# Performance work log

Hardware: AMD Instinct MI355X
Metric: run time of the kernel (lower is better)

## Reference

```python
import jax, jax.numpy as jnp
import numpy as np

HEAD_DIM = 64
N_HEADS = 25
N_KV_HEADS = 5
WINDOW = 1024
N_META = 128
EPS = 1e-6
ROPE_BASE = 10000.0


def _rmsnorm(x, w):
    # per-head RMSNorm over last dim, computed in fp32 (matches HymbaRMSNorm)
    xf = x.astype(jnp.float32)
    var = jnp.mean(xf * xf, axis=-1, keepdims=True)
    return w * (xf * jax.lax.rsqrt(var + EPS)).astype(x.dtype)


def _rotate_half(x):
    x1, x2 = jnp.split(x, 2, axis=-1)
    return jnp.concatenate((-x2, x1), axis=-1)


def _rope_cos_sin(position_ids):
    # equivalent to indexing the cached cos/sin tables with position_ids
    inv_freq = 1.0 / (ROPE_BASE ** (jnp.arange(0, HEAD_DIM, 2, dtype=jnp.float32) / HEAD_DIM))
    freqs = position_ids.astype(jnp.float32)[..., None] * inv_freq  # [B,T,hd/2]
    emb = jnp.concatenate((freqs, freqs), axis=-1)                   # [B,T,hd]
    return jnp.cos(emb)[:, None], jnp.sin(emb)[:, None]              # [B,1,T,hd]


def setup_inputs() -> dict:
    key = jax.random.key(0)
    k1, k2, k3, k4, k5 = jax.random.split(key, 5)
    B, T = 2, 2048
    return {
        "query_states": jax.random.normal(k1, (B, T, N_HEADS * HEAD_DIM), dtype=jnp.float32),
        "key_states": jax.random.normal(k2, (B, T, N_KV_HEADS * HEAD_DIM), dtype=jnp.float32),
        "value_states": jax.random.normal(k3, (B, T, N_KV_HEADS * HEAD_DIM), dtype=jnp.float32),
        "q_norm_w": jax.random.uniform(k4, (HEAD_DIM,), dtype=jnp.float32, minval=0.5, maxval=1.5),
        "k_norm_w": jax.random.uniform(k5, (HEAD_DIM,), dtype=jnp.float32, minval=0.5, maxval=1.5),
        "position_ids": jnp.broadcast_to(jnp.arange(T, dtype=jnp.int32), (B, T)),
    }


def reference(query_states, key_states, value_states, q_norm_w, k_norm_w, position_ids):
    B, T, _ = query_states.shape
    # [B, H, T, hd]
    q = query_states.reshape(B, T, N_HEADS, HEAD_DIM).transpose(0, 2, 1, 3)
    k = key_states.reshape(B, T, N_KV_HEADS, HEAD_DIM).transpose(0, 2, 1, 3)
    v = value_states.reshape(B, T, N_KV_HEADS, HEAD_DIM).transpose(0, 2, 1, 3)

    # per-head QK RMSNorm
    q = _rmsnorm(q, q_norm_w)
    k = _rmsnorm(k, k_norm_w)

    # RoPE
    cos, sin = _rope_cos_sin(position_ids)
    q = q * cos + _rotate_half(q) * sin
    k = k * cos + _rotate_half(k) * sin

    # GQA: repeat each kv head num_heads // num_kv_heads times (consecutively)
    n_rep = N_HEADS // N_KV_HEADS
    k_e = jnp.repeat(k, n_rep, axis=1)
    v_e = jnp.repeat(v, n_rep, axis=1)

    scale = 1.0 / np.sqrt(HEAD_DIM)
    scores = jnp.einsum("bhqd,bhkd->bhqk", q, k_e) * scale

    # SWA mask: causal AND (in sliding window OR meta/memory token)
    q_idx = jnp.arange(T)[:, None]
    k_idx = jnp.arange(T)[None, :]
    attend = (k_idx <= q_idx) & ((k_idx >= q_idx - WINDOW + 1) | (k_idx < N_META))
    scores = jnp.where(attend, scores, -jnp.inf)

    attn_weights = jax.nn.softmax(scores, axis=-1)
    out = jnp.einsum("bhqk,bhkd->bhqd", attn_weights, v_e)
    return out.transpose(0, 2, 1, 3).reshape(B, T, N_HEADS * HEAD_DIM)
```

## Files before the change

### kernel.cpp

```cpp
#include <hip/hip_runtime.h>
#include <cmath>

typedef float  f32x4  __attribute__((ext_vector_type(4)));
typedef __bf16 bf16x8 __attribute__((ext_vector_type(8)));
typedef unsigned int u32x4 __attribute__((ext_vector_type(4)));
typedef unsigned int u32x2 __attribute__((ext_vector_type(2)));
typedef unsigned int   u32;
typedef unsigned short u16;

#define HEAD_DIM 64
#define N_HEADS  25
#define N_KV     5
#define WINDOW   1024
#define N_META   128
#define B_       2
#define T_       2048
#define QB       64
#define NTILES   (T_ / 64)
#define TILE_U32 2048
#define SM_BIAS  (-20.0f)

static __device__ __forceinline__ u16 bf16_bits(float f) {
  __bf16 h = (__bf16)f;
  return __builtin_bit_cast(u16, h);
}
static __device__ __forceinline__ u32 pack2(float lo, float hi) {
  return ((u32)bf16_bits(hi) << 16) | bf16_bits(lo);
}
static __device__ __forceinline__ float fexp2(float x) {
  return __builtin_amdgcn_exp2f(x);
}
static __device__ __forceinline__ void gload16(const u32* g, u32* l) {
  __builtin_amdgcn_global_load_lds((const __attribute__((address_space(1))) u32*)g,
                                   (__attribute__((address_space(3))) u32*)l, 16, 0, 0);
}

__global__ __launch_bounds__(256) void prep_k_kernel(
    const float* __restrict__ k_in, const float* __restrict__ k_w,
    const int* __restrict__ pos_ids, u32* __restrict__ k_ws)
{
  int gw   = (blockIdx.x * blockDim.x + threadIdx.x) >> 6;
  int lane = threadIdx.x & 63;
  if (gw >= B_ * T_ * N_KV) return;
  int kvh = gw % N_KV;
  int bt  = gw / N_KV;

  float x = k_in[(size_t)bt * (N_KV * HEAD_DIM) + kvh * HEAD_DIM + lane];
  float ss = x * x;
  #pragma unroll
  for (int off = 32; off; off >>= 1) ss += __shfl_xor(ss, off);
  float y = k_w[lane] * x * rsqrtf(ss * (1.f / 64.f) + 1e-6f);

  int   pos = pos_ids[bt];
  float ang = (float)pos * powf(10000.f, -(float)(lane & 31) * (1.f / 32.f));
  float c, s;
  sincosf(ang, &s, &c);
  float part = __shfl_xor(y, 32);
  float r = (lane < 32) ? (y * c - part * s) : (y * c + part * s);

  u16 mybits = bf16_bits(r);
  u32 pb = (u32)(u16)__shfl_xor((int)mybits, 1);
  u32 w  = (pb << 16) | mybits;
  int b = bt / T_, t = bt % T_;
  if (!(lane & 1)) {
    int c32 = lane >> 1;
    int kl = t & 63, tile = t >> 6;
    int sp = (c32 >> 2) ^ (kl & 7);
    k_ws[(((size_t)(b * N_KV + kvh) * NTILES + tile)) * TILE_U32 + kl * 32 + sp * 4 + (c32 & 3)] = w;
  }
}

__global__ __launch_bounds__(256) void prep_v_kernel(
    const float* __restrict__ v_in, u32* __restrict__ v_ws)
{
  int blk  = blockIdx.x;
  int tile = blk & (NTILES - 1);
  int bk   = blk >> 5;
  int kvh  = bk % N_KV, b = bk / N_KV;
  int t0   = tile * 64;
  int tid  = threadIdx.x;

  __shared__ u16 Tl[64][72];

  #pragma unroll
  for (int it = 0; it < 4; ++it) {
    int idx = it * 256 + tid;
    int kl = idx >> 4, dq = idx & 15;
    const float4 f = *(const float4*)&v_in[((size_t)(b * T_ + t0 + kl)) * (N_KV * HEAD_DIM) + kvh * HEAD_DIM + dq * 4];
    Tl[dq * 4 + 0][kl] = bf16_bits(f.x);
    Tl[dq * 4 + 1][kl] = bf16_bits(f.y);
    Tl[dq * 4 + 2][kl] = bf16_bits(f.z);
    Tl[dq * 4 + 3][kl] = bf16_bits(f.w);
  }
  __syncthreads();

  u32* outb = v_ws + (size_t)blk * TILE_U32;
  #pragma unroll
  for (int it = 0; it < 8; ++it) {
    int o = it * 256 + tid;
    int d = o >> 5, c = o & 31;
    u32 w = ((u32)Tl[d][2 * c + 1] << 16) | Tl[d][2 * c];
    int a = c >> 4, bs = (c >> 3) & 1, gp = (c >> 1) & 3, e = c & 1;
    int sp = (4 * a + gp) ^ (d & 7);
    outb[d * 32 + sp * 4 + 2 * bs + e] = w;
  }
}

__global__ __launch_bounds__(256, 4) void attn_kernel(
    const float* __restrict__ q_in, const float* __restrict__ q_w,
    const int* __restrict__ pos_ids,
    const u32* __restrict__ kws, const u32* __restrict__ vws,
    float* __restrict__ out)
{
  const int i  = blockIdx.x;
  const int x  = i & 7, k = i >> 3;
  const int gA = (5 * x) >> 2;
  const int a0 = 200 * x - 160 * gA;
  const int nB = 40 + a0;
  int grp, j_;
  if (k < nB) { grp = gA + 1; j_ = k; }
  else        { grp = gA;     j_ = a0 + (k - nB); }
  const int qt  = 31 - j_ / 5;
  const int hh  = j_ % 5;
  const int b   = grp / 5;
  const int kvh = grp % 5;
  const int h   = kvh * 5 + hh;
  const int qb  = qt * QB;
  const int tid = threadIdx.x, wid = tid >> 6, lane = tid & 63;
  const int l15 = lane & 15, g = lane >> 4;
  const int qrow0 = wid * 16;

  __shared__ u32 Ks[2 * TILE_U32];
  __shared__ u32 Vt[2 * TILE_U32];

  const int nt    = (qt <= 18) ? (qt + 1) : 19;
  const int shift = qt - 18;

  const size_t kvbase = ((size_t)(b * N_KV + kvh)) * NTILES * TILE_U32;
  const u32* kb = kws + kvbase;
  const u32* vb = vws + kvbase;

  #pragma unroll
  for (int j = 0; j < 4; ++j) {
    int ci = (wid << 2) | j;
    if (ci < 8) gload16(kb + ci * 256 + lane * 4, &Ks[ci * 256]);
    else        gload16(vb + (ci - 8) * 256 + lane * 4, &Vt[(ci - 8) * 256]);
  }

  {
    const int   jbase = (4 * l15) & 31;
    const float r32   = 0.74989420933f;
    float fr[4];
    fr[0] = powf(10000.f, -(float)jbase * (1.f / 32.f));
    fr[1] = fr[0] * r32; fr[2] = fr[1] * r32; fr[3] = fr[2] * r32;

    const int t0g = b * T_ + qb + qrow0;
    int pos_prev = pos_ids[t0g + g];
    float cc[4], sn[4], c4[4], s4[4];
    #pragma unroll
    for (int e = 0; e < 4; ++e) {
      sincosf((float)pos_prev * fr[e], &sn[e], &cc[e]);
      sincosf(4.f * fr[e], &s4[e], &c4[e]);
    }
    const float4 wv = *(const float4*)&q_w[4 * l15];
    #pragma unroll
    for (int it = 0; it < 4; ++it) {
      const int row = 4 * it + g;
      if (it) {
        int pos = pos_ids[t0g + row];
        if (__all(pos == pos_prev + 4)) {
          #pragma unroll
          for (int e = 0; e < 4; ++e) {
            float c2 = cc[e] * c4[e] - sn[e] * s4[e];
            sn[e] = sn[e] * c4[e] + cc[e] * s4[e];
            cc[e] = c2;
          }
        } else {
          #pragma unroll
          for (int e = 0; e < 4; ++e) sincosf((float)pos * fr[e], &sn[e], &cc[e]);
        }
        pos_prev = pos;
      }
      const float4 xv = *(const float4*)&q_in[((size_t)(t0g + row)) * (N_HEADS * HEAD_DIM) + h * HEAD_DIM + 4 * l15];
      float ss = xv.x * xv.x + xv.y * xv.y + xv.z * xv.z + xv.w * xv.w;
      ss += __shfl_xor(ss, 1); ss += __shfl_xor(ss, 2);
      ss += __shfl_xor(ss, 4); ss += __shfl_xor(ss, 8);
      const float rn = rsqrtf(ss * (1.f / 64.f) + 1e-6f);
      float y[4] = {wv.x * xv.x * rn, wv.y * xv.y * rn, wv.z * xv.z * rn, wv.w * xv.w * rn};
      float rv[4];
      #pragma unroll
      for (int e = 0; e < 4; ++e) {
        float part = __shfl_xor(y[e], 8);
        rv[e] = ((l15 < 8) ? (y[e] * cc[e] - part * sn[e])
                           : (y[e] * cc[e] + part * sn[e])) * 0.18033688f;
      }
      u32x2 w2;
      w2.x = pack2(rv[0], rv[1]);
      w2.y = pack2(rv[2], rv[3]);
      *(u32x2*)&Ks[TILE_U32 + (qrow0 + row) * 32 + 2 * l15] = w2;
    }
  }
  __syncthreads();

  bf16x8 qf[2];
  #pragma unroll
  for (int ks = 0; ks < 2; ++ks)
    qf[ks] = *(const bf16x8*)&Ks[TILE_U32 + (qrow0 + l15) * 32 + 16 * ks + 4 * g];
  __syncthreads();

  float l_part = 0.f;
  f32x4 acc_o[4];
  #pragma unroll
  for (int mt = 0; mt < 4; ++mt) acc_o[mt] = (f32x4)(0.f);

  const int q_abs = qb + qrow0 + l15;

  int buf = 0;
  for (int i2 = 0; i2 < nt; ++i2) {
    if (i2 + 1 < nt) {
      int tn = (qt <= 18 || i2 + 1 < 2) ? (i2 + 1) : (i2 + 1 + shift);
      const u32* kt = kb + (size_t)tn * TILE_U32;
      const u32* vt = vb + (size_t)tn * TILE_U32;
      u32* kd = &Ks[(buf ^ 1) * TILE_U32];
      u32* vd = &Vt[(buf ^ 1) * TILE_U32];
      #pragma unroll
      for (int j = 0; j < 4; ++j) {
        int ci = (wid << 2) | j;
        if (ci < 8) gload16(kt + ci * 256 + lane * 4, kd + ci * 256);
        else        gload16(vt + (ci - 8) * 256 + lane * 4, vd + (ci - 8) * 256);
      }
    }
    const int k0 = ((qt <= 18 || i2 < 2) ? i2 : i2 + shift) << 6;

    f32x4 accs[4];
    #pragma unroll
    for (int mt = 0; mt < 4; ++mt) accs[mt] = (f32x4)(SM_BIAS);
    #pragma unroll
    for (int ks = 0; ks < 2; ++ks) {
      #pragma unroll
      for (int mt = 0; mt < 4; ++mt) {
        bf16x8 kf = *(const bf16x8*)&Ks[buf * TILE_U32 + (16 * mt + l15) * 32 + (((4 * ks + g) ^ (l15 & 7)) << 2)];
        accs[mt] = __builtin_amdgcn_mfma_f32_16x16x32_bf16(kf, qf[ks], accs[mt], 0, 0, 0);
      }
    }

    const bool do_mask = (i2 == nt - 1) || (qt >= 18 && i2 == 2);
    if (do_mask) {
      #pragma unroll
      for (int mt = 0; mt < 4; ++mt)
        #pragma unroll
        for (int rg = 0; rg < 4; ++rg) {
          int key = k0 + 16 * mt + 4 * g + rg;
          bool ok = (key <= q_abs) && ((key >= q_abs - (WINDOW - 1)) || (key < N_META));
          accs[mt][rg] = ok ? accs[mt][rg] : -INFINITY;
        }
    }
    float rsum = 0.f;
    #pragma unroll
    for (int mt = 0; mt < 4; ++mt)
      #pragma unroll
      for (int rg = 0; rg < 4; ++rg) {
        float pi = fexp2(accs[mt][rg]);
        accs[mt][rg] = pi;
        rsum += pi;
      }
    l_part += rsum;

    #pragma unroll
    for (int ks2 = 0; ks2 < 2; ++ks2) {
      const int m0 = 2 * ks2, m1 = 2 * ks2 + 1;
      u32x4 aw;
      aw.x = pack2(accs[m0][0], accs[m0][1]);
      aw.y = pack2(accs[m0][2], accs[m0][3]);
      aw.z = pack2(accs[m1][0], accs[m1][1]);
      aw.w = pack2(accs[m1][2], accs[m1][3]);
      bf16x8 af = __builtin_bit_cast(bf16x8, aw);
      #pragma unroll
      for (int mt2 = 0; mt2 < 4; ++mt2) {
        bf16x8 vf = *(const bf16x8*)&Vt[buf * TILE_U32 + (16 * mt2 + l15) * 32 + (((4 * ks2 + g) ^ (l15 & 7)) << 2)];
        acc_o[mt2] = __builtin_amdgcn_mfma_f32_16x16x32_bf16(af, vf, acc_o[mt2], 0, 0, 0);
      }
    }

    __syncthreads();
    buf ^= 1;
  }

  float lsum = l_part;
  lsum += __shfl_xor(lsum, 16);
  lsum += __shfl_xor(lsum, 32);
  float l4[4];
  #pragma unroll
  for (int rg = 0; rg < 4; ++rg) l4[rg] = __shfl(lsum, 4 * g + rg);
  #pragma unroll
  for (int mt2 = 0; mt2 < 4; ++mt2)
    #pragma unroll
    for (int rg = 0; rg < 4; ++rg) {
      int t = qb + qrow0 + 4 * g + rg;
      out[((size_t)(b * T_ + t)) * (N_HEADS * HEAD_DIM) + h * HEAD_DIM + 16 * mt2 + l15] =
          acc_o[mt2][rg] / l4[rg];
    }
}

extern "C" void kernel_launch(void* const* d_in, const int* in_sizes, int n_in,
                              void* d_out, int out_size, void* d_ws, size_t ws_size,
                              hipStream_t stream) {
  const float* q   = (const float*)d_in[0];
  const float* k   = (const float*)d_in[1];
  const float* v   = (const float*)d_in[2];
  const float* qw  = (const float*)d_in[3];
  const float* kw  = (const float*)d_in[4];
  const int*   pos = (const int*)d_in[5];

  u32* kp = (u32*)d_ws;
  u32* vp = kp + (size_t)B_ * N_KV * NTILES * TILE_U32;
  float* outp = (float*)d_out;

  prep_k_kernel<<<5120, 256, 0, stream>>>(k, kw, pos, kp);
  prep_v_kernel<<<B_ * N_KV * NTILES, 256, 0, stream>>>(v, vp);
  attn_kernel<<<1600, 256, 0, stream>>>(q, qw, pos, kp, vp, outp);
}
```

Measured before the change: 60.85 us.

## Split attention tile 2x2 across waves over query and key halves

Each of the four waves now handles 32 query rows against one 32-key half of each tile, instead of 16 query rows against all 64 keys. Each K fragment read from LDS is reused for two query fragments, cutting LDS reads per MFMA for the score product. The price is an end-of-kernel reduction: waves owning the second key half write partial outputs and row sums to shared memory, the other waves add them and store the result. This also raises accumulator register use.

```diff
diff --git a/kernel.cpp b/kernel.cpp
--- a/kernel.cpp
+++ b/kernel.cpp
@@ -128,7 +128,7 @@
   const int qb  = qt * QB;
   const int tid = threadIdx.x, wid = tid >> 6, lane = tid & 63;
   const int l15 = lane & 15, g = lane >> 4;
-  const int qrow0 = wid * 16;
+  const int qw  = wid >> 1, kw = wid & 1;
 
   __shared__ u32 Ks[2 * TILE_U32];
   __shared__ u32 Vt[2 * TILE_U32];
@@ -154,7 +154,7 @@
     fr[0] = powf(10000.f, -(float)jbase * (1.f / 32.f));
     fr[1] = fr[0] * r32; fr[2] = fr[1] * r32; fr[3] = fr[2] * r32;
 
-    const int t0g = b * T_ + qb + qrow0;
+    const int t0g = b * T_ + qb + wid * 16;
     int pos_prev = pos_ids[t0g + g];
     float cc[4], sn[4], c4[4], s4[4];
     #pragma unroll
@@ -197,23 +197,27 @@
       u32x2 w2;
       w2.x = pack2(rv[0], rv[1]);
       w2.y = pack2(rv[2], rv[3]);
-      *(u32x2*)&Ks[TILE_U32 + (qrow0 + row) * 32 + 2 * l15] = w2;
+      *(u32x2*)&Ks[TILE_U32 + (wid * 16 + row) * 32 + 2 * l15] = w2;
     }
   }
   __syncthreads();
 
-  bf16x8 qf[2];
-  #pragma unroll
-  for (int ks = 0; ks < 2; ++ks)
-    qf[ks] = *(const bf16x8*)&Ks[TILE_U32 + (qrow0 + l15) * 32 + 16 * ks + 4 * g];
+  bf16x8 qf[2][2];
+  #pragma unroll
+  for (int qn = 0; qn < 2; ++qn)
+    #pragma unroll
+    for (int ks = 0; ks < 2; ++ks)
+      qf[qn][ks] = *(const bf16x8*)&Ks[TILE_U32 + (32 * qw + 16 * qn + l15) * 32 + 16 * ks + 4 * g];
   __syncthreads();
 
-  float l_part = 0.f;
-  f32x4 acc_o[4];
-  #pragma unroll
-  for (int mt = 0; mt < 4; ++mt) acc_o[mt] = (f32x4)(0.f);
-
-  const int q_abs = qb + qrow0 + l15;
+  float l_part[2] = {0.f, 0.f};
+  f32x4 acc_o[2][4];
+  #pragma unroll
+  for (int qn = 0; qn < 2; ++qn)
+    #pragma unroll
+    for (int mt = 0; mt < 4; ++mt) acc_o[qn][mt] = (f32x4)(0.f);
+
+  const int q_abs0 = qb + 32 * qw + l15;
 
   int buf = 0;
   for (int i2 = 0; i2 < nt; ++i2) {
@@ -232,53 +236,61 @@
     }
     const int k0 = ((qt <= 18 || i2 < 2) ? i2 : i2 + shift) << 6;
 
-    f32x4 accs[4];
-    #pragma unroll
-    for (int mt = 0; mt < 4; ++mt) accs[mt] = (f32x4)(SM_BIAS);
+    f32x4 accs[2][2];
+    #pragma unroll
+    for (int qn = 0; qn < 2; ++qn)
+      #pragma unroll
+      for (int mt = 0; mt < 2; ++mt) accs[qn][mt] = (f32x4)(SM_BIAS);
     #pragma unroll
     for (int ks = 0; ks < 2; ++ks) {
       #pragma unroll
-      for (int mt = 0; mt < 4; ++mt) {
-        bf16x8 kf = *(const bf16x8*)&Ks[buf * TILE_U32 + (16 * mt + l15) * 32 + (((4 * ks + g) ^ (l15 & 7)) << 2)];
-        accs[mt] = __builtin_amdgcn_mfma_f32_16x16x32_bf16(kf, qf[ks], accs[mt], 0, 0, 0);
+      for (int mt = 0; mt < 2; ++mt) {
+        bf16x8 kf = *(const bf16x8*)&Ks[buf * TILE_U32 + (32 * kw + 16 * mt + l15) * 32 + (((4 * ks + g) ^ (l15 & 7)) << 2)];
+        accs[0][mt] = __builtin_amdgcn_mfma_f32_16x16x32_bf16(kf, qf[0][ks], accs[0][mt], 0, 0, 0);
+        accs[1][mt] = __builtin_amdgcn_mfma_f32_16x16x32_bf16(kf, qf[1][ks], accs[1][mt], 0, 0, 0);
       }
     }
 
     const bool do_mask = (i2 == nt - 1) || (qt >= 18 && i2 == 2);
     if (do_mask) {
       #pragma unroll
-      for (int mt = 0; mt < 4; ++mt)
+      for (int qn = 0; qn < 2; ++qn)
+        #pragma unroll
+        for (int mt = 0; mt < 2; ++mt)
+          #pragma unroll
+          for (int rg = 0; rg < 4; ++rg) {
+            int key = k0 + 32 * kw + 16 * mt + 4 * g + rg;
+            int qa  = q_abs0 + 16 * qn;
+            bool ok = (key <= qa) && ((key >= qa - (WINDOW - 1)) || (key < N_META));
+            accs[qn][mt][rg] = ok ? accs[qn][mt][rg] : -INFINITY;
+          }
+    }
+    #pragma unroll
+    for (int qn = 0; qn < 2; ++qn) {
+      float rsum = 0.f;
+      #pragma unroll
+      for (int mt = 0; mt < 2; ++mt)
         #pragma unroll
         for (int rg = 0; rg < 4; ++rg) {
-          int key = k0 + 16 * mt + 4 * g + rg;
-          bool ok = (key <= q_abs) && ((key >= q_abs - (WINDOW - 1)) || (key < N_META));
-          accs[mt][rg] = ok ? accs[mt][rg] : -INFINITY;
+          float pi = fexp2(accs[qn][mt][rg]);
+          accs[qn][mt][rg] = pi;
+          rsum += pi;
         }
-    }
-    float rsum = 0.f;
-    #pragma unroll
-    for (int mt = 0; mt < 4; ++mt)
-      #pragma unroll
-      for (int rg = 0; rg < 4; ++rg) {
-        float pi = fexp2(accs[mt][rg]);
-        accs[mt][rg] = pi;
-        rsum += pi;
-      }
-    l_part += rsum;
-
-    #pragma unroll
-    for (int ks2 = 0; ks2 < 2; ++ks2) {
-      const int m0 = 2 * ks2, m1 = 2 * ks2 + 1;
+      l_part[qn] += rsum;
+    }
+
+    #pragma unroll
+    for (int qn = 0; qn < 2; ++qn) {
       u32x4 aw;
-      aw.x = pack2(accs[m0][0], accs[m0][1]);
-      aw.y = pack2(accs[m0][2], accs[m0][3]);
-      aw.z = pack2(accs[m1][0], accs[m1][1]);
-      aw.w = pack2(accs[m1][2], accs[m1][3]);
+      aw.x = pack2(accs[qn][0][0], accs[qn][0][1]);
+      aw.y = pack2(accs[qn][0][2], accs[qn][0][3]);
+      aw.z = pack2(accs[qn][1][0], accs[qn][1][1]);
+      aw.w = pack2(accs[qn][1][2], accs[qn][1][3]);
       bf16x8 af = __builtin_bit_cast(bf16x8, aw);
       #pragma unroll
       for (int mt2 = 0; mt2 < 4; ++mt2) {
-        bf16x8 vf = *(const bf16x8*)&Vt[buf * TILE_U32 + (16 * mt2 + l15) * 32 + (((4 * ks2 + g) ^ (l15 & 7)) << 2)];
-        acc_o[mt2] = __builtin_amdgcn_mfma_f32_16x16x32_bf16(af, vf, acc_o[mt2], 0, 0, 0);
+        bf16x8 vf = *(const bf16x8*)&Vt[buf * TILE_U32 + (16 * mt2 + l15) * 32 + (((4 * kw + g) ^ (l15 & 7)) << 2)];
+        acc_o[qn][mt2] = __builtin_amdgcn_mfma_f32_16x16x32_bf16(af, vf, acc_o[qn][mt2], 0, 0, 0);
       }
     }
 
@@ -286,20 +298,51 @@
     buf ^= 1;
   }
 
-  float lsum = l_part;
-  lsum += __shfl_xor(lsum, 16);
-  lsum += __shfl_xor(lsum, 32);
-  float l4[4];
-  #pragma unroll
-  for (int rg = 0; rg < 4; ++rg) l4[rg] = __shfl(lsum, 4 * g + rg);
-  #pragma unroll
-  for (int mt2 = 0; mt2 < 4; ++mt2)
-    #pragma unroll
-    for (int rg = 0; rg < 4; ++rg) {
-      int t = qb + qrow0 + 4 * g + rg;
-      out[((size_t)(b * T_ + t)) * (N_HEADS * HEAD_DIM) + h * HEAD_DIM + 16 * mt2 + l15] =
-          acc_o[mt2][rg] / l4[rg];
-    }
+  {
+    float* xbuf = (float*)(qw ? Vt : Ks);
+    if (kw) {
+      #pragma unroll
+      for (int qn = 0; qn < 2; ++qn)
+        #pragma unroll
+        for (int mt2 = 0; mt2 < 4; ++mt2)
+          #pragma unroll
+          for (int rg = 0; rg < 4; ++rg)
+            xbuf[(qn * 16 + mt2 * 4 + rg) * 64 + lane] = acc_o[qn][mt2][rg];
+      xbuf[32 * 64 + lane] = l_part[0];
+      xbuf[33 * 64 + lane] = l_part[1];
+    }
+  }
+  __syncthreads();
+  if (kw == 0) {
+    const float* xbuf = (const float*)(qw ? Vt : Ks);
+    #pragma unroll
+    for (int qn = 0; qn < 2; ++qn)
+      #pragma unroll
+      for (int mt2 = 0; mt2 < 4; ++mt2)
+        #pragma unroll
+        for (int rg = 0; rg < 4; ++rg)
+          acc_o[qn][mt2][rg] += xbuf[(qn * 16 + mt2 * 4 + rg) * 64 + lane];
+    l_part[0] += xbuf[32 * 64 + lane];
+    l_part[1] += xbuf[33 * 64 + lane];
+
+    #pragma unroll
+    for (int qn = 0; qn < 2; ++qn) {
+      float lsum = l_part[qn];
+      lsum += __shfl_xor(lsum, 16);
+      lsum += __shfl_xor(lsum, 32);
+      float l4[4];
+      #pragma unroll
+      for (int rg = 0; rg < 4; ++rg) l4[rg] = __shfl(lsum, 4 * g + rg);
+      #pragma unroll
+      for (int mt2 = 0; mt2 < 4; ++mt2)
+        #pragma unroll
+        for (int rg = 0; rg < 4; ++rg) {
+          int t = qb + 32 * qw + 16 * qn + 4 * g + rg;
+          out[((size_t)(b * T_ + t)) * (N_HEADS * HEAD_DIM) + h * HEAD_DIM + 16 * mt2 + l15] =
+              acc_o[qn][mt2][rg] / l4[rg];
+        }
+    }
+  }
 }
 
 extern "C" void kernel_launch(void* const* d_in, const int* in_sizes, int n_in,
```

Result: no change. 61.18 us (+0.5%).
